# Kernel tuning notes

Measured on AMD Instinct MI355X. Metric: run time of the kernel, lower is better.

The kernel has to match this reference:

```python
import jax, jax.numpy as jnp
import numpy as np

POINT_DIM, VOXEL_DIM, NUM_HEADS = 3, 256, 8
HEAD_DIM = VOXEL_DIM // NUM_HEADS


def _linear_params(key, fan_in, fan_out):
    kw, kb = jax.random.split(key)
    bound = 1.0 / np.sqrt(fan_in)
    W = jax.random.uniform(kw, (fan_out, fan_in), jnp.float32, -bound, bound)
    b = jax.random.uniform(kb, (fan_out,), jnp.float32, -bound, bound)
    return W, b


def setup_inputs() -> dict:
    key = jax.random.key(0)
    ks = jax.random.split(key, 7)
    points = jax.random.normal(ks[0], (2, 4096, POINT_DIM), jnp.float32)
    voxel_features = jax.random.normal(ks[1], (2, 2048, VOXEL_DIM), jnp.float32)
    Wp, bp = _linear_params(ks[2], POINT_DIM, VOXEL_DIM)
    Wq, bq = _linear_params(ks[3], VOXEL_DIM, VOXEL_DIM)
    Wk, bk = _linear_params(ks[4], VOXEL_DIM, VOXEL_DIM)
    Wv, bv = _linear_params(ks[5], VOXEL_DIM, VOXEL_DIM)
    Wf, bf = _linear_params(ks[6], VOXEL_DIM * 2, VOXEL_DIM)
    return {
        "points": points, "voxel_features": voxel_features,
        "Wp": Wp, "bp": bp, "Wq": Wq, "bq": bq,
        "Wk": Wk, "bk": bk, "Wv": Wv, "bv": bv,
        "Wf": Wf, "bf": bf,
    }


def reference(points, voxel_features, Wp, bp, Wq, bq, Wk, bk, Wv, bv, Wf, bf):
    B, N, _ = points.shape
    M = voxel_features.shape[1]
    # projections (torch Linear: x @ W.T + b)
    point_features = points @ Wp.T + bp                      # [B,N,D]
    q = (point_features @ Wq.T + bq).reshape(B, N, NUM_HEADS, HEAD_DIM)
    k = (voxel_features @ Wk.T + bk).reshape(B, M, NUM_HEADS, HEAD_DIM)
    v = (voxel_features @ Wv.T + bv).reshape(B, M, NUM_HEADS, HEAD_DIM)
    # attention scores [B,H,N,M]
    scale = 1.0 / np.sqrt(HEAD_DIM).astype(np.float32)
    attn = jnp.einsum('bnhd,bmhd->bhnm', q, k) * scale
    attn = jax.nn.softmax(attn, axis=-1)
    attended = jnp.einsum('bhnm,bmhd->bnhd', attn, v).reshape(B, N, VOXEL_DIM)
    fused = jnp.concatenate([point_features, attended], axis=-1) @ Wf.T + bf
    return fused
```

## Files before the change

### kernel.cpp

```cpp
#include <hip/hip_runtime.h>

#define B_ 2
#define N_ 4096
#define M_ 2048
#define D_ 256
#define H_ 8
#define DH_ 32
#define ROWS_ (B_*N_)
#define KVROWS_ (B_*M_)
#define PRE_ (0.17677669529663687f * 1.4426950408889634f)
#define CBASE_ 32.0f

typedef __attribute__((ext_vector_type(8))) short short8_t;
typedef __attribute__((ext_vector_type(4))) float float4_t;

#if defined(__has_builtin)
# if __has_builtin(__builtin_amdgcn_exp2f)
#  define EXP2F(x) __builtin_amdgcn_exp2f(x)
# else
#  define EXP2F(x) exp2f(x)
# endif
#else
# define EXP2F(x) exp2f(x)
#endif

__device__ __forceinline__ unsigned int rne_u(float f) {
    union { float f; unsigned int u; } c;
    c.f = f;
    return c.u + 0x7FFFu + ((c.u >> 16) & 1u);
}

__device__ __forceinline__ unsigned short f2us(float f) {
    return (unsigned short)(rne_u(f) >> 16);
}

__device__ __forceinline__ unsigned int pack2rn(float a, float b) {
    return __builtin_amdgcn_perm(rne_u(b), rne_u(a), 0x07060302u);
}

__device__ __forceinline__ unsigned int pack2tr(float a, float b) {
    union { float f; unsigned int u; } x, y;
    x.f = a; y.f = b;
    return __builtin_amdgcn_perm(y.u, x.u, 0x07060302u);
}

__device__ __forceinline__ short8_t cvt8(float4 a, float4 b) {
    union { unsigned int u[4]; short8_t s; } c;
    c.u[0] = pack2rn(a.x, a.y);
    c.u[1] = pack2rn(a.z, a.w);
    c.u[2] = pack2rn(b.x, b.y);
    c.u[3] = pack2rn(b.z, b.w);
    return c.s;
}

__device__ __forceinline__ int xcd_swz(int bid, int nwg) {
    const int cpx = nwg >> 3;
    return (bid & 7) * cpx + (bid >> 3);
}

template<int K, int NCOL, int LDSRC>
__device__ __forceinline__ void stageB2(const float* __restrict__ W, int col0, int kof,
                                        unsigned short* __restrict__ Bs, int tid)
{
    const int n = tid & (NCOL - 1), g = tid / NCOL;
    const int GROUPS = 256 / NCOL;
    const int CPT = (K / 8) / GROUPS;
    const float* src = W + (size_t)(col0 + n) * LDSRC + kof + g * (K / GROUPS);
#pragma unroll
    for (int ci = 0; ci < CPT; ci++) {
        int logc = g * CPT + ci;
        int phys = logc ^ (n & 7);
        short8_t v = cvt8(*(const float4*)(src + ci * 8), *(const float4*)(src + ci * 8 + 4));
        *(short8_t*)(Bs + (size_t)n * K + phys * 8) = v;
    }
}

template<int K>
__device__ __forceinline__ short8_t readB(const unsigned short* __restrict__ Bs,
                                          int c, int l16, int quad, int k0)
{
    int phys = ((k0 >> 3) + quad) ^ (l16 & 7);
    return *(const short8_t*)(Bs + (size_t)(16 * c + l16) * K + phys * 8);
}

__global__ __launch_bounds__(256) void g_projkv(
    const float* __restrict__ voxel,
    const float* __restrict__ Wp, const float* __restrict__ bp,
    const float* __restrict__ Wq, const float* __restrict__ bq,
    const float* __restrict__ Wk, const float* __restrict__ bk,
    const float* __restrict__ Wv, const float* __restrict__ bv,
    const float* __restrict__ Wf, const float* __restrict__ bfb,
    unsigned short* __restrict__ k_g, unsigned short* __restrict__ vt_g,
    float* __restrict__ Wqc, float* __restrict__ Wfc)
{
    const int tid = threadIdx.x;
    const int wave = tid >> 6, lane = tid & 63, quad = lane >> 4, l16 = lane & 15;

    __shared__ unsigned short Bs[64 * 256];
    __shared__ unsigned short Bs2[64 * 256];

    if (blockIdx.x < 256) {
        const int bid = (int)blockIdx.x;
        const int row0 = (bid >> 2) * 64;
        const int col0 = (bid & 3) * 64;
        const float* arow = voxel + (size_t)(row0 + wave * 16 + l16) * D_;

        stageB2<256, 64, 256>(Wk, col0, 0, Bs, tid);
        stageB2<256, 64, 256>(Wv, col0, 0, Bs2, tid);

        float4_t ak[4], av[4];
#pragma unroll
        for (int c = 0; c < 4; c++) {
            ak[c] = (float4_t){0.f, 0.f, 0.f, 0.f};
            av[c] = (float4_t){0.f, 0.f, 0.f, 0.f};
        }
        __syncthreads();
#pragma unroll
        for (int k0 = 0; k0 < 256; k0 += 32) {
            short8_t af = cvt8(*(const float4*)(arow + k0 + quad * 8),
                               *(const float4*)(arow + k0 + quad * 8 + 4));
#pragma unroll
            for (int c = 0; c < 4; c++) {
                ak[c] = __builtin_amdgcn_mfma_f32_16x16x32_bf16(af, readB<256>(Bs,  c, l16, quad, k0), ak[c], 0, 0, 0);
                av[c] = __builtin_amdgcn_mfma_f32_16x16x32_bf16(af, readB<256>(Bs2, c, l16, quad, k0), av[c], 0, 0, 0);
            }
        }
        const int b = row0 / M_;
        const int m0 = row0 - b * M_ + wave * 16 + quad * 4;
#pragma unroll
        for (int c = 0; c < 4; c++) {
            int col = col0 + 16 * c + l16;
            float bbk = bk[col], bbv = bv[col];
#pragma unroll
            for (int r = 0; r < 4; r++) {
                int row = row0 + wave * 16 + quad * 4 + r;
                k_g[(size_t)row * D_ + col] = f2us(ak[c][r] + bbk);
            }
            int h = col >> 5, dh = col & 31;
            unsigned int u0 = pack2rn(av[c][0] + bbv, av[c][1] + bbv);
            unsigned int u1 = pack2rn(av[c][2] + bbv, av[c][3] + bbv);
            *(uint2*)(vt_g + (size_t)((b * H_ + h) * DH_ + dh) * M_ + m0) = make_uint2(u0, u1);
        }
    } else {
        const int role = (int)blockIdx.x - 256;
        float* wps = (float*)Bs;
        *(float4*)(wps + tid * 4) = make_float4(Wp[tid * 3 + 0], Wp[tid * 3 + 1],
                                                Wp[tid * 3 + 2], bp[tid]);
        __syncthreads();
        const int col = tid;
        const float* wrow = role ? (Wf + (size_t)col * 512) : (Wq + (size_t)col * 256);
        float a0 = 0.f, a1 = 0.f, a2 = 0.f, ab = 0.f;
#pragma unroll 4
        for (int d = 0; d < 256; d += 4) {
            float4 wv = *(const float4*)(wrow + d);
            float4 w0 = *(const float4*)(wps + (d + 0) * 4);
            float4 w1 = *(const float4*)(wps + (d + 1) * 4);
            float4 w2 = *(const float4*)(wps + (d + 2) * 4);
            float4 w3 = *(const float4*)(wps + (d + 3) * 4);
            a0 += wv.x * w0.x + wv.y * w1.x + wv.z * w2.x + wv.w * w3.x;
            a1 += wv.x * w0.y + wv.y * w1.y + wv.z * w2.y + wv.w * w3.y;
            a2 += wv.x * w0.z + wv.y * w1.z + wv.z * w2.z + wv.w * w3.z;
            ab += wv.x * w0.w + wv.y * w1.w + wv.z * w2.w + wv.w * w3.w;
        }
        if (role == 0) {
            *(float4*)(Wqc + (size_t)col * 4) =
                make_float4(a0 * PRE_, a1 * PRE_, a2 * PRE_, (ab + bq[col]) * PRE_);
        } else {
            *(float4*)(Wfc + (size_t)col * 4) =
                make_float4(a0, a1, a2, ab + bfb[col]);
        }
    }
}

__global__ __launch_bounds__(256) void k_attn9(
    const float* __restrict__ points, const float* __restrict__ Wqc,
    const unsigned short* __restrict__ k_g,
    const unsigned short* __restrict__ vt_g,
    unsigned short* __restrict__ att_g)
{
    const int tid = threadIdx.x;
    const int w = tid >> 6, lane = tid & 63, quad = lane >> 4, l16 = lane & 15;
    const int lbid = xcd_swz((int)blockIdx.x, B_ * H_ * (N_ / 64));
    const int nt = lbid & 63;
    const int bh = lbid >> 6;
    const int b = bh >> 3, h = bh & 7;
    const int n0 = nt * 64 + w * 16;

    __shared__ unsigned short Kt[2][64][40];
    __shared__ unsigned short Vt[2][32][72];

    const unsigned short* kbase = k_g + (size_t)(b * M_) * D_ + h * DH_;
    const unsigned short* vbase = vt_g + (size_t)(bh * DH_) * M_;

    const int kr = tid >> 2, kc = tid & 3;
    const int vr = tid >> 3, vc = tid & 7;
    const int ksr = kr ^ ((kr & 8) >> 1);

    const unsigned short* kq = kbase + (size_t)kr * D_ + kc * 8;
    const unsigned short* vq = vbase + (size_t)vr * M_ + vc * 8;

    *(short8_t*)&Kt[0][ksr][kc * 8] = *(const short8_t*)kq;
    *(short8_t*)&Vt[0][vr][vc * 8] = *(const short8_t*)vq;

    const int rbas = 8 * (l16 >> 2) + (l16 & 3);
    const int rx = l16 & 4;
    int krow[4];
#pragma unroll
    for (int t = 0; t < 4; t++)
        krow[t] = (rbas + 4 * (t & 1) + 32 * (t >> 1)) ^ rx;

    const size_t qrow = (size_t)(b * N_ + n0 + l16);
    const float p0 = points[qrow * 3 + 0];
    const float p1 = points[qrow * 3 + 1];
    const float p2 = points[qrow * 3 + 2];
    float q8[8];
#pragma unroll
    for (int j = 0; j < 8; j++) {
        float4 wc = *(const float4*)(Wqc + (size_t)(h * DH_ + quad * 8 + j) * 4);
        q8[j] = p0 * wc.x + p1 * wc.y + p2 * wc.z + wc.w;
    }
    short8_t qf = cvt8(make_float4(q8[0], q8[1], q8[2], q8[3]),
                       make_float4(q8[4], q8[5], q8[6], q8[7]));

    float4_t od0 = {0.f, 0.f, 0.f, 0.f};
    float4_t od1 = {0.f, 0.f, 0.f, 0.f};
    float l_lane = 0.f;

    const float4_t zc = {-CBASE_, -CBASE_, -CBASE_, -CBASE_};

#pragma unroll 2
    for (int s = 0; s < M_ / 64; s++) {
        __syncthreads();
        const int buf = s & 1;
        const bool more = (s + 1 < M_ / 64);
        short8_t knext, vnext;
        if (more) {
            kq += 64 * D_;
            vq += 64;
            knext = *(const short8_t*)kq;
            vnext = *(const short8_t*)vq;
        }

        float4_t st[4];
#pragma unroll
        for (int t = 0; t < 4; t++) {
            short8_t kf = *(const short8_t*)&Kt[buf][krow[t]][quad * 8];
            st[t] = __builtin_amdgcn_mfma_f32_16x16x32_bf16(kf, qf, zc, 0, 0, 0);
        }

        float psum = 0.f;
        unsigned int uu[4][2];
#pragma unroll
        for (int t = 0; t < 4; t++) {
            float p0e = EXP2F(st[t][0]);
            float p1e = EXP2F(st[t][1]);
            float p2e = EXP2F(st[t][2]);
            float p3e = EXP2F(st[t][3]);
            psum += (p0e + p1e) + (p2e + p3e);
            uu[t][0] = pack2tr(p0e, p1e);
            uu[t][1] = pack2tr(p2e, p3e);
        }
        l_lane += psum;

        union { unsigned int u[4]; short8_t s; } pa, pb2;
        pa.u[0]  = uu[0][0]; pa.u[1]  = uu[0][1]; pa.u[2]  = uu[1][0]; pa.u[3]  = uu[1][1];
        pb2.u[0] = uu[2][0]; pb2.u[1] = uu[2][1]; pb2.u[2] = uu[3][0]; pb2.u[3] = uu[3][1];

        short8_t vf00 = *(const short8_t*)&Vt[buf][l16][quad * 8];
        short8_t vf01 = *(const short8_t*)&Vt[buf][l16][32 + quad * 8];
        short8_t vf10 = *(const short8_t*)&Vt[buf][16 + l16][quad * 8];
        short8_t vf11 = *(const short8_t*)&Vt[buf][16 + l16][32 + quad * 8];
        od0 = __builtin_amdgcn_mfma_f32_16x16x32_bf16(vf00, pa.s,  od0, 0, 0, 0);
        od0 = __builtin_amdgcn_mfma_f32_16x16x32_bf16(vf01, pb2.s, od0, 0, 0, 0);
        od1 = __builtin_amdgcn_mfma_f32_16x16x32_bf16(vf10, pa.s,  od1, 0, 0, 0);
        od1 = __builtin_amdgcn_mfma_f32_16x16x32_bf16(vf11, pb2.s, od1, 0, 0, 0);

        if (more) {
            *(short8_t*)&Kt[buf ^ 1][ksr][kc * 8] = knext;
            *(short8_t*)&Vt[buf ^ 1][vr][vc * 8] = vnext;
        }
    }

    l_lane += __shfl_xor(l_lane, 16);
    l_lane += __shfl_xor(l_lane, 32);
    const float inv = 1.0f / l_lane;

    unsigned short* ob = att_g + (size_t)(b * N_ + n0 + l16) * D_ + h * DH_;
    {
        unsigned int u0 = pack2rn(od0[0] * inv, od0[1] * inv);
        unsigned int u1 = pack2rn(od0[2] * inv, od0[3] * inv);
        *(uint2*)(ob + quad * 4) = make_uint2(u0, u1);
        unsigned int u2 = pack2rn(od1[0] * inv, od1[1] * inv);
        unsigned int u3 = pack2rn(od1[2] * inv, od1[3] * inv);
        *(uint2*)(ob + 16 + quad * 4) = make_uint2(u2, u3);
    }
}

__global__ __launch_bounds__(256) void g_fuse2(
    const unsigned short* __restrict__ att_g,
    const float* __restrict__ points, const float* __restrict__ Wfc,
    const float* __restrict__ Wf,
    float* __restrict__ out)
{
    const int tid = threadIdx.x;
    const int wave = tid >> 6, lane = tid & 63, quad = lane >> 4, l16 = lane & 15;
    const int lbid = xcd_swz((int)blockIdx.x, (ROWS_ / 64) * 8);
    const int row0 = (lbid >> 3) * 64;
    const int col0 = (lbid & 7) * 32;

    __shared__ unsigned short Bs[32 * 256];

    stageB2<256, 32, 512>(Wf, col0, 256, Bs, tid);
    __syncthreads();

    float4_t acc[2];
#pragma unroll
    for (int c = 0; c < 2; c++) acc[c] = (float4_t){0.f, 0.f, 0.f, 0.f};

    const size_t arow = (size_t)(row0 + wave * 16 + l16) * D_;
#pragma unroll
    for (int k0 = 0; k0 < 256; k0 += 32) {
        short8_t af = *(const short8_t*)(att_g + arow + k0 + quad * 8);
#pragma unroll
        for (int c = 0; c < 2; c++)
            acc[c] = __builtin_amdgcn_mfma_f32_16x16x32_bf16(af, readB<256>(Bs, c, l16, quad, k0), acc[c], 0, 0, 0);
    }

    const int rbase = row0 + wave * 16 + quad * 4;
    float px[4], py[4], pz[4];
#pragma unroll
    for (int r = 0; r < 4; r++) {
        px[r] = points[(size_t)(rbase + r) * 3 + 0];
        py[r] = points[(size_t)(rbase + r) * 3 + 1];
        pz[r] = points[(size_t)(rbase + r) * 3 + 2];
    }
#pragma unroll
    for (int c = 0; c < 2; c++) {
        int col = col0 + 16 * c + l16;
        float4 wf = *(const float4*)(Wfc + (size_t)col * 4);
#pragma unroll
        for (int r = 0; r < 4; r++) {
            out[(size_t)(rbase + r) * D_ + col] =
                acc[c][r] + px[r] * wf.x + py[r] * wf.y + pz[r] * wf.z + wf.w;
        }
    }
}

extern "C" void kernel_launch(void* const* d_in, const int* in_sizes, int n_in,
                              void* d_out, int out_size, void* d_ws, size_t ws_size,
                              hipStream_t stream)
{
    const float* points = (const float*)d_in[0];
    const float* voxel  = (const float*)d_in[1];
    const float* Wp  = (const float*)d_in[2];
    const float* bp  = (const float*)d_in[3];
    const float* Wq  = (const float*)d_in[4];
    const float* bq  = (const float*)d_in[5];
    const float* Wk  = (const float*)d_in[6];
    const float* bk  = (const float*)d_in[7];
    const float* Wv  = (const float*)d_in[8];
    const float* bv  = (const float*)d_in[9];
    const float* Wf  = (const float*)d_in[10];
    const float* bfb = (const float*)d_in[11];
    float* out = (float*)d_out;

    float* Wqc = (float*)d_ws;
    float* Wfc = Wqc + 256 * 4;
    unsigned short* k_g   = (unsigned short*)(Wfc + 256 * 4);
    unsigned short* vt_g  = k_g  + (size_t)KVROWS_ * D_;
    unsigned short* att_g = vt_g + (size_t)KVROWS_ * D_;

    g_projkv<<<dim3(258),  dim3(256), 0, stream>>>(voxel, Wp, bp, Wq, bq, Wk, bk,
                                                   Wv, bv, Wf, bfb, k_g, vt_g, Wqc, Wfc);
    k_attn9 <<<dim3(B_ * H_ * (N_ / 64)), dim3(256), 0, stream>>>(points, Wqc, k_g, vt_g, att_g);
    g_fuse2 <<<dim3((ROWS_ / 64) * 8), dim3(256), 0, stream>>>(att_g, points, Wfc, Wf, out);
}
```

Baseline: 134.9 us.

## Fuse three kernels into one persistent kernel with global barriers

Replaces the three separate launches (projection, attention, fuse) with a single 1024-block kernel that runs each phase in turn, separated by atomic-counter grid barriers, plus a memset to reset the counters. The projection phase is re-tiled into 32x32 tiles spread across all 1024 blocks, and the Wq/Wf collapse into the point projection now uses per-wave shuffle reductions instead of two dedicated blocks. The aim is to remove launch gaps and tail effects between kernels. In exchange it depends on all 1024 blocks being co-resident (4 per CU under the launch bounds), otherwise the barriers deadlock, and it adds spin-wait and fence overhead.

```diff
diff --git a/kernel.cpp b/kernel.cpp
--- a/kernel.cpp
+++ b/kernel.cpp
@@ -8,6 +8,7 @@
 #define DH_ 32
 #define ROWS_ (B_*N_)
 #define KVROWS_ (B_*M_)
+#define NBLK_ 1024
 #define PRE_ (0.17677669529663687f * 1.4426950408889634f)
 #define CBASE_ 32.0f
 
@@ -83,114 +84,131 @@
     return *(const short8_t*)(Bs + (size_t)(16 * c + l16) * K + phys * 8);
 }
 
-__global__ __launch_bounds__(256) void g_projkv(
-    const float* __restrict__ voxel,
-    const float* __restrict__ Wp, const float* __restrict__ bp,
-    const float* __restrict__ Wq, const float* __restrict__ bq,
-    const float* __restrict__ Wk, const float* __restrict__ bk,
-    const float* __restrict__ Wv, const float* __restrict__ bv,
-    const float* __restrict__ Wf, const float* __restrict__ bfb,
-    unsigned short* __restrict__ k_g, unsigned short* __restrict__ vt_g,
-    float* __restrict__ Wqc, float* __restrict__ Wfc)
-{
-    const int tid = threadIdx.x;
-    const int wave = tid >> 6, lane = tid & 63, quad = lane >> 4, l16 = lane & 15;
-
-    __shared__ unsigned short Bs[64 * 256];
-    __shared__ unsigned short Bs2[64 * 256];
-
-    if (blockIdx.x < 256) {
-        const int bid = (int)blockIdx.x;
-        const int row0 = (bid >> 2) * 64;
-        const int col0 = (bid & 3) * 64;
-        const float* arow = voxel + (size_t)(row0 + wave * 16 + l16) * D_;
-
-        stageB2<256, 64, 256>(Wk, col0, 0, Bs, tid);
-        stageB2<256, 64, 256>(Wv, col0, 0, Bs2, tid);
-
-        float4_t ak[4], av[4];
-#pragma unroll
-        for (int c = 0; c < 4; c++) {
-            ak[c] = (float4_t){0.f, 0.f, 0.f, 0.f};
-            av[c] = (float4_t){0.f, 0.f, 0.f, 0.f};
-        }
-        __syncthreads();
-#pragma unroll
-        for (int k0 = 0; k0 < 256; k0 += 32) {
-            short8_t af = cvt8(*(const float4*)(arow + k0 + quad * 8),
-                               *(const float4*)(arow + k0 + quad * 8 + 4));
-#pragma unroll
-            for (int c = 0; c < 4; c++) {
-                ak[c] = __builtin_amdgcn_mfma_f32_16x16x32_bf16(af, readB<256>(Bs,  c, l16, quad, k0), ak[c], 0, 0, 0);
-                av[c] = __builtin_amdgcn_mfma_f32_16x16x32_bf16(af, readB<256>(Bs2, c, l16, quad, k0), av[c], 0, 0, 0);
+struct P_t {
+    const float *points, *voxel, *Wp, *bp, *Wq, *bq, *Wk, *bk, *Wv, *bv, *Wf, *bfb;
+    unsigned short *k_g, *vt_g, *att_g;
+    float *Wqc, *Wfc, *out;
+    unsigned int *sem;
+};
+
+__device__ __forceinline__ void gbar(unsigned int* sem, int idx) {
+    __syncthreads();
+    if (threadIdx.x == 0) {
+        __threadfence();
+        atomicAdd(&sem[idx], 1u);
+        while (__hip_atomic_load(&sem[idx], __ATOMIC_RELAXED,
+                                 __HIP_MEMORY_SCOPE_AGENT) < (unsigned)NBLK_) {
+            __builtin_amdgcn_s_sleep(8);
+        }
+        __threadfence();
+    }
+    __syncthreads();
+}
+
+__device__ __forceinline__ void phase_proj(int bid, int tid,
+                                           unsigned short* __restrict__ S, const P_t& p)
+{
+    const int w = tid >> 6, lane = tid & 63, quad = lane >> 4, l16 = lane & 15;
+    const int row0 = (bid >> 3) * 32;
+    const int col0 = (bid & 7) * 32;
+
+    unsigned short* BsK = S;
+    unsigned short* BsV = S + 8192;
+
+    stageB2<256, 32, 256>(p.Wk, col0, 0, BsK, tid);
+    stageB2<256, 32, 256>(p.Wv, col0, 0, BsV, tid);
+
+    const int myrow = row0 + (w & 1) * 16 + l16;
+    const float* arow = p.voxel + (size_t)myrow * D_;
+    short8_t af[8];
+#pragma unroll
+    for (int i = 0; i < 8; i++)
+        af[i] = cvt8(*(const float4*)(arow + i * 32 + quad * 8),
+                     *(const float4*)(arow + i * 32 + quad * 8 + 4));
+
+    const unsigned short* ws = (w >> 1) ? BsV : BsK;
+    float4_t acc[2];
+#pragma unroll
+    for (int c = 0; c < 2; c++) acc[c] = (float4_t){0.f, 0.f, 0.f, 0.f};
+    __syncthreads();
+#pragma unroll
+    for (int i = 0; i < 8; i++)
+#pragma unroll
+        for (int c = 0; c < 2; c++)
+            acc[c] = __builtin_amdgcn_mfma_f32_16x16x32_bf16(af[i], readB<256>(ws, c, l16, quad, i * 32), acc[c], 0, 0, 0);
+
+    if (w < 2) {
+#pragma unroll
+        for (int c = 0; c < 2; c++) {
+            int col = col0 + 16 * c + l16;
+            float bbk = p.bk[col];
+#pragma unroll
+            for (int r = 0; r < 4; r++) {
+                int row = row0 + (w & 1) * 16 + quad * 4 + r;
+                p.k_g[(size_t)row * D_ + col] = f2us(acc[c][r] + bbk);
             }
         }
+    } else {
         const int b = row0 / M_;
-        const int m0 = row0 - b * M_ + wave * 16 + quad * 4;
-#pragma unroll
-        for (int c = 0; c < 4; c++) {
+        const int m0 = row0 - b * M_ + (w & 1) * 16 + quad * 4;
+#pragma unroll
+        for (int c = 0; c < 2; c++) {
             int col = col0 + 16 * c + l16;
-            float bbk = bk[col], bbv = bv[col];
-#pragma unroll
-            for (int r = 0; r < 4; r++) {
-                int row = row0 + wave * 16 + quad * 4 + r;
-                k_g[(size_t)row * D_ + col] = f2us(ak[c][r] + bbk);
-            }
+            float bbv = p.bv[col];
             int h = col >> 5, dh = col & 31;
-            unsigned int u0 = pack2rn(av[c][0] + bbv, av[c][1] + bbv);
-            unsigned int u1 = pack2rn(av[c][2] + bbv, av[c][3] + bbv);
-            *(uint2*)(vt_g + (size_t)((b * H_ + h) * DH_ + dh) * M_ + m0) = make_uint2(u0, u1);
-        }
-    } else {
-        const int role = (int)blockIdx.x - 256;
-        float* wps = (float*)Bs;
-        *(float4*)(wps + tid * 4) = make_float4(Wp[tid * 3 + 0], Wp[tid * 3 + 1],
-                                                Wp[tid * 3 + 2], bp[tid]);
-        __syncthreads();
-        const int col = tid;
-        const float* wrow = role ? (Wf + (size_t)col * 512) : (Wq + (size_t)col * 256);
+            unsigned int u0 = pack2rn(acc[c][0] + bbv, acc[c][1] + bbv);
+            unsigned int u1 = pack2rn(acc[c][2] + bbv, acc[c][3] + bbv);
+            *(uint2*)(p.vt_g + (size_t)((b * H_ + h) * DH_ + dh) * M_ + m0) = make_uint2(u0, u1);
+        }
+    }
+
+    if (bid < 512 && w == 0) {
+        const int col = bid & 255;
+        const bool isQ = (bid < 256);
+        const float* wrow = isQ ? (p.Wq + (size_t)col * 256) : (p.Wf + (size_t)col * 512);
         float a0 = 0.f, a1 = 0.f, a2 = 0.f, ab = 0.f;
-#pragma unroll 4
-        for (int d = 0; d < 256; d += 4) {
-            float4 wv = *(const float4*)(wrow + d);
-            float4 w0 = *(const float4*)(wps + (d + 0) * 4);
-            float4 w1 = *(const float4*)(wps + (d + 1) * 4);
-            float4 w2 = *(const float4*)(wps + (d + 2) * 4);
-            float4 w3 = *(const float4*)(wps + (d + 3) * 4);
-            a0 += wv.x * w0.x + wv.y * w1.x + wv.z * w2.x + wv.w * w3.x;
-            a1 += wv.x * w0.y + wv.y * w1.y + wv.z * w2.y + wv.w * w3.y;
-            a2 += wv.x * w0.z + wv.y * w1.z + wv.z * w2.z + wv.w * w3.z;
-            ab += wv.x * w0.w + wv.y * w1.w + wv.z * w2.w + wv.w * w3.w;
-        }
-        if (role == 0) {
-            *(float4*)(Wqc + (size_t)col * 4) =
-                make_float4(a0 * PRE_, a1 * PRE_, a2 * PRE_, (ab + bq[col]) * PRE_);
-        } else {
-            *(float4*)(Wfc + (size_t)col * 4) =
-                make_float4(a0, a1, a2, ab + bfb[col]);
-        }
-    }
-}
-
-__global__ __launch_bounds__(256) void k_attn9(
-    const float* __restrict__ points, const float* __restrict__ Wqc,
-    const unsigned short* __restrict__ k_g,
-    const unsigned short* __restrict__ vt_g,
-    unsigned short* __restrict__ att_g)
-{
-    const int tid = threadIdx.x;
+#pragma unroll
+        for (int i = 0; i < 4; i++) {
+            int t = i * 64 + lane;
+            float wv = wrow[t];
+            a0 += wv * p.Wp[t * 3 + 0];
+            a1 += wv * p.Wp[t * 3 + 1];
+            a2 += wv * p.Wp[t * 3 + 2];
+            ab += wv * p.bp[t];
+        }
+#pragma unroll
+        for (int m = 1; m < 64; m <<= 1) {
+            a0 += __shfl_xor(a0, m);
+            a1 += __shfl_xor(a1, m);
+            a2 += __shfl_xor(a2, m);
+            ab += __shfl_xor(ab, m);
+        }
+        if (lane == 0) {
+            if (isQ)
+                *(float4*)(p.Wqc + (size_t)col * 4) =
+                    make_float4(a0 * PRE_, a1 * PRE_, a2 * PRE_, (ab + p.bq[col]) * PRE_);
+            else
+                *(float4*)(p.Wfc + (size_t)col * 4) =
+                    make_float4(a0, a1, a2, ab + p.bfb[col]);
+        }
+    }
+}
+
+__device__ __forceinline__ void phase_attn(int bid, int tid,
+                                           unsigned short* __restrict__ S, const P_t& p)
+{
     const int w = tid >> 6, lane = tid & 63, quad = lane >> 4, l16 = lane & 15;
-    const int lbid = xcd_swz((int)blockIdx.x, B_ * H_ * (N_ / 64));
+    const int lbid = xcd_swz(bid, NBLK_);
     const int nt = lbid & 63;
     const int bh = lbid >> 6;
     const int b = bh >> 3, h = bh & 7;
     const int n0 = nt * 64 + w * 16;
 
-    __shared__ unsigned short Kt[2][64][40];
-    __shared__ unsigned short Vt[2][32][72];
-
-    const unsigned short* kbase = k_g + (size_t)(b * M_) * D_ + h * DH_;
-    const unsigned short* vbase = vt_g + (size_t)(bh * DH_) * M_;
+    unsigned short* Kt = S;
+    unsigned short* Vt = S + 5120;
+
+    const unsigned short* kbase = p.k_g + (size_t)(b * M_) * D_ + h * DH_;
+    const unsigned short* vbase = p.vt_g + (size_t)(bh * DH_) * M_;
 
     const int kr = tid >> 2, kc = tid & 3;
     const int vr = tid >> 3, vc = tid & 7;
@@ -199,8 +217,8 @@
     const unsigned short* kq = kbase + (size_t)kr * D_ + kc * 8;
     const unsigned short* vq = vbase + (size_t)vr * M_ + vc * 8;
 
-    *(short8_t*)&Kt[0][ksr][kc * 8] = *(const short8_t*)kq;
-    *(short8_t*)&Vt[0][vr][vc * 8] = *(const short8_t*)vq;
+    *(short8_t*)(Kt + ksr * 40 + kc * 8) = *(const short8_t*)kq;
+    *(short8_t*)(Vt + vr * 72 + vc * 8) = *(const short8_t*)vq;
 
     const int rbas = 8 * (l16 >> 2) + (l16 & 3);
     const int rx = l16 & 4;
@@ -210,13 +228,13 @@
         krow[t] = (rbas + 4 * (t & 1) + 32 * (t >> 1)) ^ rx;
 
     const size_t qrow = (size_t)(b * N_ + n0 + l16);
-    const float p0 = points[qrow * 3 + 0];
-    const float p1 = points[qrow * 3 + 1];
-    const float p2 = points[qrow * 3 + 2];
+    const float p0 = p.points[qrow * 3 + 0];
+    const float p1 = p.points[qrow * 3 + 1];
+    const float p2 = p.points[qrow * 3 + 2];
     float q8[8];
 #pragma unroll
     for (int j = 0; j < 8; j++) {
-        float4 wc = *(const float4*)(Wqc + (size_t)(h * DH_ + quad * 8 + j) * 4);
+        float4 wc = *(const float4*)(p.Wqc + (size_t)(h * DH_ + quad * 8 + j) * 4);
         q8[j] = p0 * wc.x + p1 * wc.y + p2 * wc.z + wc.w;
     }
     short8_t qf = cvt8(make_float4(q8[0], q8[1], q8[2], q8[3]),
@@ -244,7 +262,7 @@
         float4_t st[4];
 #pragma unroll
         for (int t = 0; t < 4; t++) {
-            short8_t kf = *(const short8_t*)&Kt[buf][krow[t]][quad * 8];
+            short8_t kf = *(const short8_t*)(Kt + buf * 2560 + krow[t] * 40 + quad * 8);
             st[t] = __builtin_amdgcn_mfma_f32_16x16x32_bf16(kf, qf, zc, 0, 0, 0);
         }
 
@@ -266,18 +284,18 @@
         pa.u[0]  = uu[0][0]; pa.u[1]  = uu[0][1]; pa.u[2]  = uu[1][0]; pa.u[3]  = uu[1][1];
         pb2.u[0] = uu[2][0]; pb2.u[1] = uu[2][1]; pb2.u[2] = uu[3][0]; pb2.u[3] = uu[3][1];
 
-        short8_t vf00 = *(const short8_t*)&Vt[buf][l16][quad * 8];
-        short8_t vf01 = *(const short8_t*)&Vt[buf][l16][32 + quad * 8];
-        short8_t vf10 = *(const short8_t*)&Vt[buf][16 + l16][quad * 8];
-        short8_t vf11 = *(const short8_t*)&Vt[buf][16 + l16][32 + quad * 8];
+        short8_t vf00 = *(const short8_t*)(Vt + buf * 2304 + l16 * 72 + quad * 8);
+        short8_t vf01 = *(const short8_t*)(Vt + buf * 2304 + l16 * 72 + 32 + quad * 8);
+        short8_t vf10 = *(const short8_t*)(Vt + buf * 2304 + (16 + l16) * 72 + quad * 8);
+        short8_t vf11 = *(const short8_t*)(Vt + buf * 2304 + (16 + l16) * 72 + 32 + quad * 8);
         od0 = __builtin_amdgcn_mfma_f32_16x16x32_bf16(vf00, pa.s,  od0, 0, 0, 0);
         od0 = __builtin_amdgcn_mfma_f32_16x16x32_bf16(vf01, pb2.s, od0, 0, 0, 0);
         od1 = __builtin_amdgcn_mfma_f32_16x16x32_bf16(vf10, pa.s,  od1, 0, 0, 0);
         od1 = __builtin_amdgcn_mfma_f32_16x16x32_bf16(vf11, pb2.s, od1, 0, 0, 0);
 
         if (more) {
-            *(short8_t*)&Kt[buf ^ 1][ksr][kc * 8] = knext;
-            *(short8_t*)&Vt[buf ^ 1][vr][vc * 8] = vnext;
+            *(short8_t*)(Kt + (buf ^ 1) * 2560 + ksr * 40 + kc * 8) = knext;
+            *(short8_t*)(Vt + (buf ^ 1) * 2304 + vr * 72 + vc * 8) = vnext;
         }
     }
 
@@ -285,7 +303,7 @@
     l_lane += __shfl_xor(l_lane, 32);
     const float inv = 1.0f / l_lane;
 
-    unsigned short* ob = att_g + (size_t)(b * N_ + n0 + l16) * D_ + h * DH_;
+    unsigned short* ob = p.att_g + (size_t)(b * N_ + n0 + l16) * D_ + h * DH_;
     {
         unsigned int u0 = pack2rn(od0[0] * inv, od0[1] * inv);
         unsigned int u1 = pack2rn(od0[2] * inv, od0[3] * inv);
@@ -296,21 +314,15 @@
     }
 }
 
-__global__ __launch_bounds__(256) void g_fuse2(
-    const unsigned short* __restrict__ att_g,
-    const float* __restrict__ points, const float* __restrict__ Wfc,
-    const float* __restrict__ Wf,
-    float* __restrict__ out)
-{
-    const int tid = threadIdx.x;
+__device__ __forceinline__ void phase_fuse(int bid, int tid,
+                                           unsigned short* __restrict__ S, const P_t& p)
+{
     const int wave = tid >> 6, lane = tid & 63, quad = lane >> 4, l16 = lane & 15;
-    const int lbid = xcd_swz((int)blockIdx.x, (ROWS_ / 64) * 8);
+    const int lbid = xcd_swz(bid, NBLK_);
     const int row0 = (lbid >> 3) * 64;
     const int col0 = (lbid & 7) * 32;
 
-    __shared__ unsigned short Bs[32 * 256];
-
-    stageB2<256, 32, 512>(Wf, col0, 256, Bs, tid);
+    stageB2<256, 32, 512>(p.Wf, col0, 256, S, tid);
     __syncthreads();
 
     float4_t acc[2];
@@ -320,58 +332,70 @@
     const size_t arow = (size_t)(row0 + wave * 16 + l16) * D_;
 #pragma unroll
     for (int k0 = 0; k0 < 256; k0 += 32) {
-        short8_t af = *(const short8_t*)(att_g + arow + k0 + quad * 8);
+        short8_t af = *(const short8_t*)(p.att_g + arow + k0 + quad * 8);
 #pragma unroll
         for (int c = 0; c < 2; c++)
-            acc[c] = __builtin_amdgcn_mfma_f32_16x16x32_bf16(af, readB<256>(Bs, c, l16, quad, k0), acc[c], 0, 0, 0);
+            acc[c] = __builtin_amdgcn_mfma_f32_16x16x32_bf16(af, readB<256>(S, c, l16, quad, k0), acc[c], 0, 0, 0);
     }
 
     const int rbase = row0 + wave * 16 + quad * 4;
     float px[4], py[4], pz[4];
 #pragma unroll
     for (int r = 0; r < 4; r++) {
-        px[r] = points[(size_t)(rbase + r) * 3 + 0];
-        py[r] = points[(size_t)(rbase + r) * 3 + 1];
-        pz[r] = points[(size_t)(rbase + r) * 3 + 2];
+        px[r] = p.points[(size_t)(rbase + r) * 3 + 0];
+        py[r] = p.points[(size_t)(rbase + r) * 3 + 1];
+        pz[r] = p.points[(size_t)(rbase + r) * 3 + 2];
     }
 #pragma unroll
     for (int c = 0; c < 2; c++) {
         int col = col0 + 16 * c + l16;
-        float4 wf = *(const float4*)(Wfc + (size_t)col * 4);
+        float4 wf = *(const float4*)(p.Wfc + (size_t)col * 4);
 #pragma unroll
         for (int r = 0; r < 4; r++) {
-            out[(size_t)(rbase + r) * D_ + col] =
+            p.out[(size_t)(rbase + r) * D_ + col] =
                 acc[c][r] + px[r] * wf.x + py[r] * wf.y + pz[r] * wf.z + wf.w;
         }
     }
+}
+
+__global__ __launch_bounds__(256, 4) void k_fused(P_t p)
+{
+    __shared__ __align__(16) unsigned short S[16384];
+    const int bid = (int)blockIdx.x, tid = (int)threadIdx.x;
+
+    phase_proj(bid, tid, S, p);
+    gbar(p.sem, 0);
+    phase_attn(bid, tid, S, p);
+    gbar(p.sem, 1);
+    phase_fuse(bid, tid, S, p);
 }
 
 extern "C" void kernel_launch(void* const* d_in, const int* in_sizes, int n_in,
                               void* d_out, int out_size, void* d_ws, size_t ws_size,
                               hipStream_t stream)
 {
-    const float* points = (const float*)d_in[0];
-    const float* voxel  = (const float*)d_in[1];
-    const float* Wp  = (const float*)d_in[2];
-    const float* bp  = (const float*)d_in[3];
-    const float* Wq  = (const float*)d_in[4];
-    const float* bq  = (const float*)d_in[5];
-    const float* Wk  = (const float*)d_in[6];
-    const float* bk  = (const float*)d_in[7];
-    const float* Wv  = (const float*)d_in[8];
-    const float* bv  = (const float*)d_in[9];
-    const float* Wf  = (const float*)d_in[10];
-    const float* bfb = (const float*)d_in[11];
-    float* out = (float*)d_out;
-
-    float* Wqc = (float*)d_ws;
-    float* Wfc = Wqc + 256 * 4;
-    unsigned short* k_g   = (unsigned short*)(Wfc + 256 * 4);
-    unsigned short* vt_g  = k_g  + (size_t)KVROWS_ * D_;
-    unsigned short* att_g = vt_g + (size_t)KVROWS_ * D_;
-
-    g_projkv<<<dim3(258),  dim3(256), 0, stream>>>(voxel, Wp, bp, Wq, bq, Wk, bk,
-                                                   Wv, bv, Wf, bfb, k_g, vt_g, Wqc, Wfc);
-    k_attn9 <<<dim3(B_ * H_ * (N_ / 64)), dim3(256), 0, stream>>>(points, Wqc, k_g, vt_g, att_g);
-    g_fuse2 <<<dim3((ROWS_ / 64) * 8), dim3(256), 0, stream>>>(att_g, points, Wfc, Wf, out);
-}
+    P_t p;
+    p.points = (const float*)d_in[0];
+    p.voxel  = (const float*)d_in[1];
+    p.Wp  = (const float*)d_in[2];
+    p.bp  = (const float*)d_in[3];
+    p.Wq  = (const float*)d_in[4];
+    p.bq  = (const float*)d_in[5];
+    p.Wk  = (const float*)d_in[6];
+    p.bk  = (const float*)d_in[7];
+    p.Wv  = (const float*)d_in[8];
+    p.bv  = (const float*)d_in[9];
+    p.Wf  = (const float*)d_in[10];
+    p.bfb = (const float*)d_in[11];
+    p.out = (float*)d_out;
+
+    p.sem = (unsigned int*)d_ws;
+    p.Wqc = (float*)d_ws + 16;
+    p.Wfc = p.Wqc + 256 * 4;
+    p.k_g   = (unsigned short*)(p.Wfc + 256 * 4);
+    p.vt_g  = p.k_g  + (size_t)KVROWS_ * D_;
+    p.att_g = p.vt_g + (size_t)KVROWS_ * D_;
+
+    hipMemsetAsync(d_ws, 0, 64, stream);
+    k_fused<<<dim3(NBLK_), dim3(256), 0, stream>>>(p);
+}
```

Result: slower. 398.7 us (+195.5%).

## Retile K/V projection, attention, and fuse kernels for more parallelism and reuse

Applied to the files above, without the earlier changes.

The K/V projection kernel now splits K and V into separate blocks (512 blocks instead of 256), which halves shared memory per block, preloads the activation row fragments, and adds XCD swizzling. The attention kernel processes 128 query rows per 512-thread block, so each K/V tile staged in LDS serves twice as many queries. K and V loads are split across thread halves. The fuse kernel widens column tiles from 32 to 64 to reuse A fragments. The trade-off is fewer attention blocks and heavier fuse blocks, and each voxel row is now read twice in the projection kernel.

```diff
diff --git a/kernel.cpp b/kernel.cpp
--- a/kernel.cpp
+++ b/kernel.cpp
@@ -83,7 +83,7 @@
     return *(const short8_t*)(Bs + (size_t)(16 * c + l16) * K + phys * 8);
 }
 
-__global__ __launch_bounds__(256) void g_projkv(
+__global__ __launch_bounds__(256) void g_projkv4(
     const float* __restrict__ voxel,
     const float* __restrict__ Wp, const float* __restrict__ bp,
     const float* __restrict__ Wq, const float* __restrict__ bq,
@@ -97,52 +97,60 @@
     const int wave = tid >> 6, lane = tid & 63, quad = lane >> 4, l16 = lane & 15;
 
     __shared__ unsigned short Bs[64 * 256];
-    __shared__ unsigned short Bs2[64 * 256];
-
-    if (blockIdx.x < 256) {
-        const int bid = (int)blockIdx.x;
-        const int row0 = (bid >> 2) * 64;
-        const int col0 = (bid & 3) * 64;
+
+    const int bid = (int)blockIdx.x;
+    if (bid < 512) {
+        const int lbid = xcd_swz(bid, 512);
+        const int row0 = (lbid >> 3) * 64;
+        const int sub  = lbid & 7;
+        const int col0 = (sub >> 1) * 64;
+        const bool isV = sub & 1;
+
+        stageB2<256, 64, 256>(isV ? Wv : Wk, col0, 0, Bs, tid);
+
         const float* arow = voxel + (size_t)(row0 + wave * 16 + l16) * D_;
-
-        stageB2<256, 64, 256>(Wk, col0, 0, Bs, tid);
-        stageB2<256, 64, 256>(Wv, col0, 0, Bs2, tid);
-
-        float4_t ak[4], av[4];
-#pragma unroll
-        for (int c = 0; c < 4; c++) {
-            ak[c] = (float4_t){0.f, 0.f, 0.f, 0.f};
-            av[c] = (float4_t){0.f, 0.f, 0.f, 0.f};
-        }
+        short8_t af[8];
+#pragma unroll
+        for (int i = 0; i < 8; i++)
+            af[i] = cvt8(*(const float4*)(arow + i * 32 + quad * 8),
+                         *(const float4*)(arow + i * 32 + quad * 8 + 4));
+
+        float4_t acc[4];
+#pragma unroll
+        for (int c = 0; c < 4; c++) acc[c] = (float4_t){0.f, 0.f, 0.f, 0.f};
         __syncthreads();
 #pragma unroll
-        for (int k0 = 0; k0 < 256; k0 += 32) {
-            short8_t af = cvt8(*(const float4*)(arow + k0 + quad * 8),
-                               *(const float4*)(arow + k0 + quad * 8 + 4));
+        for (int i = 0; i < 8; i++)
+#pragma unroll
+            for (int c = 0; c < 4; c++)
+                acc[c] = __builtin_amdgcn_mfma_f32_16x16x32_bf16(af[i], readB<256>(Bs, c, l16, quad, i * 32), acc[c], 0, 0, 0);
+
+        if (!isV) {
 #pragma unroll
             for (int c = 0; c < 4; c++) {
-                ak[c] = __builtin_amdgcn_mfma_f32_16x16x32_bf16(af, readB<256>(Bs,  c, l16, quad, k0), ak[c], 0, 0, 0);
-                av[c] = __builtin_amdgcn_mfma_f32_16x16x32_bf16(af, readB<256>(Bs2, c, l16, quad, k0), av[c], 0, 0, 0);
+                int col = col0 + 16 * c + l16;
+                float bbk = bk[col];
+#pragma unroll
+                for (int r = 0; r < 4; r++) {
+                    int row = row0 + wave * 16 + quad * 4 + r;
+                    k_g[(size_t)row * D_ + col] = f2us(acc[c][r] + bbk);
+                }
             }
-        }
-        const int b = row0 / M_;
-        const int m0 = row0 - b * M_ + wave * 16 + quad * 4;
-#pragma unroll
-        for (int c = 0; c < 4; c++) {
-            int col = col0 + 16 * c + l16;
-            float bbk = bk[col], bbv = bv[col];
-#pragma unroll
-            for (int r = 0; r < 4; r++) {
-                int row = row0 + wave * 16 + quad * 4 + r;
-                k_g[(size_t)row * D_ + col] = f2us(ak[c][r] + bbk);
+        } else {
+            const int b = row0 / M_;
+            const int m0 = row0 - b * M_ + wave * 16 + quad * 4;
+#pragma unroll
+            for (int c = 0; c < 4; c++) {
+                int col = col0 + 16 * c + l16;
+                float bbv = bv[col];
+                int h = col >> 5, dh = col & 31;
+                unsigned int u0 = pack2rn(acc[c][0] + bbv, acc[c][1] + bbv);
+                unsigned int u1 = pack2rn(acc[c][2] + bbv, acc[c][3] + bbv);
+                *(uint2*)(vt_g + (size_t)((b * H_ + h) * DH_ + dh) * M_ + m0) = make_uint2(u0, u1);
             }
-            int h = col >> 5, dh = col & 31;
-            unsigned int u0 = pack2rn(av[c][0] + bbv, av[c][1] + bbv);
-            unsigned int u1 = pack2rn(av[c][2] + bbv, av[c][3] + bbv);
-            *(uint2*)(vt_g + (size_t)((b * H_ + h) * DH_ + dh) * M_ + m0) = make_uint2(u0, u1);
         }
     } else {
-        const int role = (int)blockIdx.x - 256;
+        const int role = bid - 512;
         float* wps = (float*)Bs;
         *(float4*)(wps + tid * 4) = make_float4(Wp[tid * 3 + 0], Wp[tid * 3 + 1],
                                                 Wp[tid * 3 + 2], bp[tid]);
@@ -172,7 +180,7 @@
     }
 }
 
-__global__ __launch_bounds__(256) void k_attn9(
+__global__ __launch_bounds__(512) void k_attn10(
     const float* __restrict__ points, const float* __restrict__ Wqc,
     const unsigned short* __restrict__ k_g,
     const unsigned short* __restrict__ vt_g,
@@ -180,11 +188,11 @@
 {
     const int tid = threadIdx.x;
     const int w = tid >> 6, lane = tid & 63, quad = lane >> 4, l16 = lane & 15;
-    const int lbid = xcd_swz((int)blockIdx.x, B_ * H_ * (N_ / 64));
-    const int nt = lbid & 63;
-    const int bh = lbid >> 6;
+    const int lbid = xcd_swz((int)blockIdx.x, B_ * H_ * (N_ / 128));
+    const int nt = lbid & 31;
+    const int bh = lbid >> 5;
     const int b = bh >> 3, h = bh & 7;
-    const int n0 = nt * 64 + w * 16;
+    const int n0 = nt * 128 + w * 16;
 
     __shared__ unsigned short Kt[2][64][40];
     __shared__ unsigned short Vt[2][32][72];
@@ -192,15 +200,19 @@
     const unsigned short* kbase = k_g + (size_t)(b * M_) * D_ + h * DH_;
     const unsigned short* vbase = vt_g + (size_t)(bh * DH_) * M_;
 
+    const bool isK = (tid < 256);
     const int kr = tid >> 2, kc = tid & 3;
-    const int vr = tid >> 3, vc = tid & 7;
+    const int vr = (tid - 256) >> 3, vc = tid & 7;
     const int ksr = kr ^ ((kr & 8) >> 1);
 
-    const unsigned short* kq = kbase + (size_t)kr * D_ + kc * 8;
-    const unsigned short* vq = vbase + (size_t)vr * M_ + vc * 8;
-
-    *(short8_t*)&Kt[0][ksr][kc * 8] = *(const short8_t*)kq;
-    *(short8_t*)&Vt[0][vr][vc * 8] = *(const short8_t*)vq;
+    const unsigned short* gq = isK ? (kbase + (size_t)kr * D_ + kc * 8)
+                                   : (vbase + (size_t)vr * M_ + vc * 8);
+    const int gstep = isK ? 64 * D_ : 64;
+    unsigned short* ldst = isK ? (&Kt[0][0][0] + ksr * 40 + kc * 8)
+                               : (&Vt[0][0][0] + vr * 72 + vc * 8);
+    const int lstride = isK ? 2560 : 2304;
+
+    *(short8_t*)ldst = *(const short8_t*)gq;
 
     const int rbas = 8 * (l16 >> 2) + (l16 & 3);
     const int rx = l16 & 4;
@@ -233,12 +245,10 @@
         __syncthreads();
         const int buf = s & 1;
         const bool more = (s + 1 < M_ / 64);
-        short8_t knext, vnext;
+        short8_t nxt;
         if (more) {
-            kq += 64 * D_;
-            vq += 64;
-            knext = *(const short8_t*)kq;
-            vnext = *(const short8_t*)vq;
+            gq += gstep;
+            nxt = *(const short8_t*)gq;
         }
 
         float4_t st[4];
@@ -275,10 +285,8 @@
         od1 = __builtin_amdgcn_mfma_f32_16x16x32_bf16(vf10, pa.s,  od1, 0, 0, 0);
         od1 = __builtin_amdgcn_mfma_f32_16x16x32_bf16(vf11, pb2.s, od1, 0, 0, 0);
 
-        if (more) {
-            *(short8_t*)&Kt[buf ^ 1][ksr][kc * 8] = knext;
-            *(short8_t*)&Vt[buf ^ 1][vr][vc * 8] = vnext;
-        }
+        if (more)
+            *(short8_t*)(ldst + (buf ^ 1) * lstride) = nxt;
     }
 
     l_lane += __shfl_xor(l_lane, 16);
@@ -296,7 +304,7 @@
     }
 }
 
-__global__ __launch_bounds__(256) void g_fuse2(
+__global__ __launch_bounds__(256) void g_fuse3(
     const unsigned short* __restrict__ att_g,
     const float* __restrict__ points, const float* __restrict__ Wfc,
     const float* __restrict__ Wf,
@@ -304,25 +312,25 @@
 {
     const int tid = threadIdx.x;
     const int wave = tid >> 6, lane = tid & 63, quad = lane >> 4, l16 = lane & 15;
-    const int lbid = xcd_swz((int)blockIdx.x, (ROWS_ / 64) * 8);
-    const int row0 = (lbid >> 3) * 64;
-    const int col0 = (lbid & 7) * 32;
-
-    __shared__ unsigned short Bs[32 * 256];
-
-    stageB2<256, 32, 512>(Wf, col0, 256, Bs, tid);
+    const int lbid = xcd_swz((int)blockIdx.x, (ROWS_ / 64) * 4);
+    const int row0 = (lbid >> 2) * 64;
+    const int col0 = (lbid & 3) * 64;
+
+    __shared__ unsigned short Bs[64 * 256];
+
+    stageB2<256, 64, 512>(Wf, col0, 256, Bs, tid);
     __syncthreads();
 
-    float4_t acc[2];
-#pragma unroll
-    for (int c = 0; c < 2; c++) acc[c] = (float4_t){0.f, 0.f, 0.f, 0.f};
+    float4_t acc[4];
+#pragma unroll
+    for (int c = 0; c < 4; c++) acc[c] = (float4_t){0.f, 0.f, 0.f, 0.f};
 
     const size_t arow = (size_t)(row0 + wave * 16 + l16) * D_;
 #pragma unroll
     for (int k0 = 0; k0 < 256; k0 += 32) {
         short8_t af = *(const short8_t*)(att_g + arow + k0 + quad * 8);
 #pragma unroll
-        for (int c = 0; c < 2; c++)
+        for (int c = 0; c < 4; c++)
             acc[c] = __builtin_amdgcn_mfma_f32_16x16x32_bf16(af, readB<256>(Bs, c, l16, quad, k0), acc[c], 0, 0, 0);
     }
 
@@ -335,7 +343,7 @@
         pz[r] = points[(size_t)(rbase + r) * 3 + 2];
     }
 #pragma unroll
-    for (int c = 0; c < 2; c++) {
+    for (int c = 0; c < 4; c++) {
         int col = col0 + 16 * c + l16;
         float4 wf = *(const float4*)(Wfc + (size_t)col * 4);
 #pragma unroll
@@ -370,8 +378,8 @@
     unsigned short* vt_g  = k_g  + (size_t)KVROWS_ * D_;
     unsigned short* att_g = vt_g + (size_t)KVROWS_ * D_;
 
-    g_projkv<<<dim3(258),  dim3(256), 0, stream>>>(voxel, Wp, bp, Wq, bq, Wk, bk,
+    g_projkv4<<<dim3(514), dim3(256), 0, stream>>>(voxel, Wp, bp, Wq, bq, Wk, bk,
                                                    Wv, bv, Wf, bfb, k_g, vt_g, Wqc, Wfc);
-    k_attn9 <<<dim3(B_ * H_ * (N_ / 64)), dim3(256), 0, stream>>>(points, Wqc, k_g, vt_g, att_g);
-    g_fuse2 <<<dim3((ROWS_ / 64) * 8), dim3(256), 0, stream>>>(att_g, points, Wfc, Wf, out);
-}
+    k_attn10<<<dim3(B_ * H_ * (N_ / 128)), dim3(512), 0, stream>>>(points, Wqc, k_g, vt_g, att_g);
+    g_fuse3 <<<dim3((ROWS_ / 64) * 4), dim3(256), 0, stream>>>(att_g, points, Wfc, Wf, out);
+}
```

Result: no change. 133.9 us (-0.8%).
